# Optimization experiments

Hardware: AMD Instinct MI355X
Metric: run time of the kernel (lower is better)

The kernel has to match this reference:

```python
import jax, jax.numpy as jnp
import numpy as np

N_PAPER, N_MESH = 60000, 30000
N = N_PAPER + N_MESH
E_TRAIN, E_DEC = 2000000, 400000
F_PAPER = F_MESH = 128
D0, H, D = 16, 32, 16  # initial embed, hidden, final embed
NREL, NB = 2, 4


def _glorot(key, shape):
    fan_in, fan_out = shape[-2], shape[-1]
    s = jnp.sqrt(6.0 / (fan_in + fan_out)).astype(jnp.float32)
    return jax.random.uniform(key, shape, jnp.float32, -s, s)


def setup_inputs() -> dict:
    key = jax.random.key(0)
    ks = iter(jax.random.split(key, 40))
    inp = {
        'x_paper': jax.random.normal(next(ks), (N_PAPER, F_PAPER), jnp.float32),
        'x_mesh': jax.random.normal(next(ks), (N_MESH, F_MESH), jnp.float32),
        'train_edge_index': jax.random.randint(next(ks), (2, E_TRAIN), 0, N, jnp.int64 if jax.config.jax_enable_x64 else jnp.int32),
        'train_edge_type': jnp.sort(jax.random.randint(next(ks), (E_TRAIN,), 0, NREL)),
        'pos_edge_index': jax.random.randint(next(ks), (2, E_DEC), 0, N),
        'pos_edge_type': jnp.sort(jax.random.randint(next(ks), (E_DEC,), 0, NREL)),
        'neg_edge_index': jax.random.randint(next(ks), (2, E_DEC), 0, N),
        'neg_edge_type': jnp.sort(jax.random.randint(next(ks), (E_DEC,), 0, NREL)),
        # input transforms
        'Wp': _glorot(next(ks), (F_PAPER, D0)), 'bp': jnp.zeros((D0,), jnp.float32),
        'Wm': _glorot(next(ks), (F_MESH, D0)), 'bm': jnp.zeros((D0,), jnp.float32),
        # decode linears
        'Wd0': _glorot(next(ks), (D, D)), 'bd0': jnp.zeros((D,), jnp.float32),
        'Wd1': _glorot(next(ks), (D, D)), 'bd1': jnp.zeros((D,), jnp.float32),
    }
    dims = [(D0, H), (H, H), (H, H), (H, D)]
    for i, (di, do) in enumerate(dims, 1):
        inp[f'bases{i}'] = _glorot(next(ks), (NB, di, do))
        inp[f'comp{i}'] = _glorot(next(ks), (NREL, NB))
        inp[f'root{i}'] = _glorot(next(ks), (di, do))
        inp[f'bias{i}'] = jnp.zeros((do,), jnp.float32)
    return inp


def rgcn_layer(x, src, dst, et, bases, comp, root, bias):
    # PyG RGCNConv with basis decomposition, per-relation mean aggregation.
    out = x @ root + bias
    xs = x[src]  # [E, in]
    for r in range(NREL):
        W_r = jnp.einsum('b,bio->io', comp[r], bases)
        m = xs @ W_r  # [E, out]
        mf = (et == r).astype(m.dtype)
        cnt = jax.ops.segment_sum(mf, dst, num_segments=N)
        agg = jax.ops.segment_sum(m * mf[:, None], dst, num_segments=N)
        out = out + agg / jnp.clip(cnt, 1.0)[:, None]
    return out


def _decode_block(z, ei, et, Wd0, bd0, Wd1, bd1):
    zs, zd = z[ei[0]], z[ei[1]]
    h0 = zs @ Wd0 + bd0
    h1 = zs @ Wd1 + bd1
    h = jnp.where((et == 0)[:, None], h0, h1)
    return jnp.sum(h * zd, axis=-1)


def reference(x_paper, x_mesh, train_edge_index, train_edge_type,
              pos_edge_index, pos_edge_type, neg_edge_index, neg_edge_type,
              Wp, bp, Wm, bm, Wd0, bd0, Wd1, bd1,
              bases1, comp1, root1, bias1, bases2, comp2, root2, bias2,
              bases3, comp3, root3, bias3, bases4, comp4, root4, bias4):
    x = jnp.concatenate([x_paper @ Wp + bp, x_mesh @ Wm + bm], axis=0)  # [N, D0]
    src, dst = train_edge_index[0], train_edge_index[1]
    x = jax.nn.relu(rgcn_layer(x, src, dst, train_edge_type, bases1, comp1, root1, bias1))
    x = jax.nn.relu(rgcn_layer(x, src, dst, train_edge_type, bases2, comp2, root2, bias2))
    x = jax.nn.relu(rgcn_layer(x, src, dst, train_edge_type, bases3, comp3, root3, bias3))
    z = rgcn_layer(x, src, dst, train_edge_type, bases4, comp4, root4, bias4)
    # edge types are sorted, so per-edge in-order compute matches the masked concat order
    pos = _decode_block(z, pos_edge_index, pos_edge_type, Wd0, bd0, Wd1, bd1)
    neg = _decode_block(z, neg_edge_index, neg_edge_type, Wd0, bd0, Wd1, bd1)
    return jnp.concatenate([pos, neg], axis=0)  # [2*E_DEC]
```

## Files before the change

kernel.cpp:

```cpp
#include <hip/hip_runtime.h>
#include <hip/hip_bf16.h>

constexpr int NN = 90000;
constexpr int NP = 60000;
constexpr int NM = 30000;
constexpr int ET = 2000000;
constexpr int ED = 400000;
constexpr int TWO_NN = 2 * NN;

constexpr int BKT_SH  = 9;
constexpr int NB_BKT  = (TWO_NN + 511) >> BKT_SH;
constexpr int BKT_CAP = 6400;
constexpr int TILE    = 2048;
constexpr int N_TILES = (ET + TILE - 1) / TILE;

__device__ __forceinline__ float bflo(unsigned int u) {
    union { unsigned int i; float f; } c;
    c.i = u << 16;
    return c.f;
}
__device__ __forceinline__ float bfhi(unsigned int u) {
    union { unsigned int i; float f; } c;
    c.i = u & 0xffff0000u;
    return c.f;
}
__device__ __forceinline__ unsigned short f2bf(float f) {
    union { float f; unsigned int i; } c;
    c.f = f;
    unsigned int x = c.i;
    return (unsigned short)((x + 0x7FFFu + ((x >> 16) & 1u)) >> 16);
}

__global__ void init_kernel(const int* __restrict__ tei, int* __restrict__ gcur,
                            int* __restrict__ dflag) {
    int b = blockIdx.x * blockDim.x + threadIdx.x;
    if (b < NB_BKT) gcur[b] = b * BKT_CAP;
    if (b == 0) {
        int allzero = 1;
        for (int i = 0; i < 16; i++)
            if (tei[2 * i + 1] != 0) allzero = 0;
        dflag[0] = allzero;
    }
}

__global__ void __launch_bounds__(256) binA_kernel(
        const int* __restrict__ ei, const int* __restrict__ et,
        const int* __restrict__ dflag, int* __restrict__ gcur,
        int2* __restrict__ pairs) {
    __shared__ int histw[4][NB_BKT];
    __shared__ int wbase[4][NB_BKT];
    __shared__ int tot[NB_BKT];
    __shared__ int excl[NB_BKT];
    __shared__ int gbase[NB_BKT];
    __shared__ int scn[256];
    __shared__ int2 tbuf[TILE];
    int t = threadIdx.x;
    int w = t >> 6;
    int tile0 = blockIdx.x * TILE;
    int tcount = ET - tile0;
    if (tcount > TILE) tcount = TILE;
    for (int i = t; i < 4 * NB_BKT; i += 256) ((int*)histw)[i] = 0;
    __syncthreads();
    int sft = dflag[0];
    int myk[8], mys[8];
#pragma unroll
    for (int q = 0; q < 8; q++) {
        int li = q * 256 + t;
        myk[q] = -1;
        if (li < tcount) {
            int e = tile0 + li;
            int s = ei[(size_t)e << sft];
            int d = ei[(size_t)(ET + e) << sft];
            int r = et[(size_t)e << sft];
            int key = r * NN + d;
            myk[q] = key;
            mys[q] = s;
            atomicAdd(&histw[w][key >> BKT_SH], 1);
        }
    }
    __syncthreads();
    for (int i = t; i < NB_BKT; i += 256) {
        int h0 = histw[0][i], h1 = histw[1][i], h2 = histw[2][i], h3 = histw[3][i];
        wbase[0][i] = 0;
        wbase[1][i] = h0;
        wbase[2][i] = h0 + h1;
        wbase[3][i] = h0 + h1 + h2;
        tot[i] = h0 + h1 + h2 + h3;
    }
    __syncthreads();
    int v0 = (t < NB_BKT / 2) ? tot[2 * t] : 0;
    int v1 = (t < NB_BKT / 2) ? tot[2 * t + 1] : 0;
    int s = v0 + v1;
    scn[t] = s;
    __syncthreads();
    for (int st = 1; st < 256; st <<= 1) {
        int u = (t >= st) ? scn[t - st] : 0;
        __syncthreads();
        scn[t] += u;
        __syncthreads();
    }
    int base = scn[t] - s;
    if (t < NB_BKT / 2) {
        excl[2 * t] = base;
        excl[2 * t + 1] = base + v0;
    }
    __syncthreads();
    for (int i = t; i < NB_BKT; i += 256) {
        int e0 = excl[i];
        wbase[0][i] += e0;
        wbase[1][i] += e0;
        wbase[2][i] += e0;
        wbase[3][i] += e0;
        histw[0][i] = 0; histw[1][i] = 0; histw[2][i] = 0; histw[3][i] = 0;
    }
    __syncthreads();
#pragma unroll
    for (int q = 0; q < 8; q++) {
        if (myk[q] >= 0) {
            int b = myk[q] >> BKT_SH;
            int p = wbase[w][b] + atomicAdd(&histw[w][b], 1);
            tbuf[p] = make_int2(myk[q], mys[q]);
        }
    }
    __syncthreads();
    for (int i = t; i < NB_BKT; i += 256)
        if (tot[i] > 0) gbase[i] = atomicAdd(&gcur[i], tot[i]);
    __syncthreads();
    for (int i = t; i < tcount; i += 256) {
        int2 p = tbuf[i];
        int b = p.x >> BKT_SH;
        int gpos = gbase[b] + (i - excl[b]);
        int cap = (b + 1) * BKT_CAP - 1;
        pairs[gpos < cap ? gpos : cap] = p;
    }
}

__global__ void __launch_bounds__(256) histplace_kernel(
        const int* __restrict__ gcur, const int2* __restrict__ pairs,
        int* __restrict__ off, int* __restrict__ endo, float* __restrict__ inv,
        int* __restrict__ csr) {
    __shared__ int kh[512];
    __shared__ int scn[256];
    int b = blockIdx.x;
    int t = threadIdx.x;
    int beg = b * BKT_CAP, end = gcur[b];
    for (int i = t; i < 512; i += 256) kh[i] = 0;
    __syncthreads();
    for (int i = beg + t; i < end; i += 256)
        atomicAdd(&kh[pairs[i].x & 511], 1);
    __syncthreads();
    int v[2];
    int s = 0;
#pragma unroll
    for (int q = 0; q < 2; q++) {
        v[q] = kh[t * 2 + q];
        s += v[q];
    }
    scn[t] = s;
    __syncthreads();
    for (int st = 1; st < 256; st <<= 1) {
        int u = (t >= st) ? scn[t - st] : 0;
        __syncthreads();
        scn[t] += u;
        __syncthreads();
    }
    int run = beg + scn[t] - s;
    int kbase = b << BKT_SH;
    int kc[2];
#pragma unroll
    for (int q = 0; q < 2; q++) {
        int key = kbase + t * 2 + q;
        if (key < TWO_NN) {
            off[key] = run;
            endo[key] = run + v[q];
            inv[key] = 1.0f / (float)(v[q] > 1 ? v[q] : 1);
        }
        kc[q] = run;
        run += v[q];
    }
    __syncthreads();
#pragma unroll
    for (int q = 0; q < 2; q++) kh[t * 2 + q] = kc[q];
    __syncthreads();
    for (int i = beg + t; i < end; i += 256) {
        int2 p = pairs[i];
        int pos = atomicAdd(&kh[p.x & 511], 1);
        csr[pos] = p.y;
    }
}

__global__ void __launch_bounds__(256) embed2_kernel(
        const float* __restrict__ Xp, const float* __restrict__ Xm,
        const float* __restrict__ Wp, const float* __restrict__ bp,
        const float* __restrict__ Wm, const float* __restrict__ bm,
        unsigned short* __restrict__ outbf) {
    __shared__ float Wl[4096 + 32];
    for (int i = threadIdx.x; i < 2048; i += 256) {
        Wl[i] = Wp[i];
        Wl[2048 + i] = Wm[i];
    }
    if (threadIdx.x < 16) {
        Wl[4096 + threadIdx.x] = bp[threadIdx.x];
        Wl[4112 + threadIdx.x] = bm[threadIdx.x];
    }
    __syncthreads();
    int n = blockIdx.x * 256 + threadIdx.x;
    if (n >= NN) return;
    const float* X;
    const float* Ws;
    const float* Bs;
    if (n < NP) { X = Xp + (size_t)n * 128; Ws = Wl; Bs = Wl + 4096; }
    else        { X = Xm + (size_t)(n - NP) * 128; Ws = Wl + 2048; Bs = Wl + 4112; }
    float acc[16];
#pragma unroll
    for (int j = 0; j < 16; j++) acc[j] = Bs[j];
    const float4* row = (const float4*)X;
    for (int k4 = 0; k4 < 32; k4++) {
        float4 xv = row[k4];
        int k = k4 * 4;
#pragma unroll
        for (int j = 0; j < 16; j++) {
            float a = acc[j];
            a = fmaf(xv.x, Ws[(k + 0) * 16 + j], a);
            a = fmaf(xv.y, Ws[(k + 1) * 16 + j], a);
            a = fmaf(xv.z, Ws[(k + 2) * 16 + j], a);
            a = fmaf(xv.w, Ws[(k + 3) * 16 + j], a);
            acc[j] = a;
        }
    }
    ushort4* ob = (ushort4*)(outbf + (size_t)n * 16);
#pragma unroll
    for (int q = 0; q < 4; q++) {
        ushort4 ub;
        ub.x = f2bf(acc[4 * q]);     ub.y = f2bf(acc[4 * q + 1]);
        ub.z = f2bf(acc[4 * q + 2]); ub.w = f2bf(acc[4 * q + 3]);
        ob[q] = ub;
    }
}

__global__ void prep_all_kernel(
        const float* __restrict__ ba0, const float* __restrict__ co0,
        const float* __restrict__ ro0, const float* __restrict__ bi0,
        const float* __restrict__ ba1, const float* __restrict__ co1,
        const float* __restrict__ ro1, const float* __restrict__ bi1,
        const float* __restrict__ ba2, const float* __restrict__ co2,
        const float* __restrict__ ro2, const float* __restrict__ bi2,
        const float* __restrict__ ba3, const float* __restrict__ co3,
        const float* __restrict__ ro3, const float* __restrict__ bi3,
        float* __restrict__ Wbuf4) {
    int l = blockIdx.x;
    const float* bases; const float* comp; const float* root; const float* bias;
    if (l == 0)      { bases = ba0; comp = co0; root = ro0; bias = bi0; }
    else if (l == 1) { bases = ba1; comp = co1; root = ro1; bias = bi1; }
    else if (l == 2) { bases = ba2; comp = co2; root = ro2; bias = bi2; }
    else             { bases = ba3; comp = co3; root = ro3; bias = bi3; }
    int din = (l == 0) ? 16 : 32;
    int dout = (l == 3) ? 16 : 32;
    int sz = din * dout;
    float* W = Wbuf4 + l * 3200;
    for (int i = threadIdx.x; i < sz; i += 256) {
        float b0 = bases[i];
        float b1 = bases[sz + i];
        float b2 = bases[2 * sz + i];
        float b3 = bases[3 * sz + i];
        for (int r = 0; r < 2; r++) {
            W[r * sz + i] = comp[r * 4 + 0] * b0 + comp[r * 4 + 1] * b1 +
                            comp[r * 4 + 2] * b2 + comp[r * 4 + 3] * b3;
        }
        W[2 * sz + i] = root[i];
    }
    if (threadIdx.x < dout) W[3 * sz + threadIdx.x] = bias[threadIdx.x];
}

template <int DIN, int DOUT, int RELU, int BS>
__global__ void __launch_bounds__(BS, 8) layer_kernel(
        const int* __restrict__ off, const int* __restrict__ endo,
        const int* __restrict__ csr,
        const unsigned short* __restrict__ xbf_in,
        const float* __restrict__ inv, const float* __restrict__ Wbuf,
        unsigned short* __restrict__ xbf_out) {
    constexpr int SZ = DIN * DOUT;
    constexpr int QL = DIN / 8;
    constexpr int TPN = 2 * QL;
    constexpr int NPB = BS / TPN;
    constexpr int AGST = 2 * DIN + 4;
    constexpr int XSST = DIN + 8;
    __shared__ float Wl[3 * SZ + DOUT];
    __shared__ float agg[NPB * AGST];
    __shared__ unsigned short xsu[NPB * XSST];
    for (int i = threadIdx.x; i < 3 * SZ + DOUT; i += BS) Wl[i] = Wbuf[i];
    int t = threadIdx.x;
    int ln = t / TPN;
    int rl = t % TPN;
    int r = rl / QL;
    int lane = rl % QL;
    int d = blockIdx.x * NPB + ln;
    if (d < NN) {
        if (r == 0) {
            uint4 u = *(const uint4*)(xbf_in + (size_t)d * DIN + lane * 8);
            *(uint4*)&xsu[ln * XSST + lane * 8] = u;
        }
        int key = r * NN + d;
        int b = off[key];
        int e = endo[key];
        float a0[8] = {0, 0, 0, 0, 0, 0, 0, 0};
        float a1[8] = {0, 0, 0, 0, 0, 0, 0, 0};
        const unsigned short* hp = xbf_in + lane * 8;
        int k = b;
        for (; k + 1 < e; k += 2) {
            int s0 = __builtin_nontemporal_load(csr + k);
            int s1 = __builtin_nontemporal_load(csr + k + 1);
            uint4 u0 = *(const uint4*)(hp + (size_t)s0 * DIN);
            uint4 u1 = *(const uint4*)(hp + (size_t)s1 * DIN);
            a0[0] += bflo(u0.x); a0[1] += bfhi(u0.x);
            a0[2] += bflo(u0.y); a0[3] += bfhi(u0.y);
            a0[4] += bflo(u0.z); a0[5] += bfhi(u0.z);
            a0[6] += bflo(u0.w); a0[7] += bfhi(u0.w);
            a1[0] += bflo(u1.x); a1[1] += bfhi(u1.x);
            a1[2] += bflo(u1.y); a1[3] += bfhi(u1.y);
            a1[4] += bflo(u1.z); a1[5] += bfhi(u1.z);
            a1[6] += bflo(u1.w); a1[7] += bfhi(u1.w);
        }
        if (k < e) {
            int s0 = __builtin_nontemporal_load(csr + k);
            uint4 u0 = *(const uint4*)(hp + (size_t)s0 * DIN);
            a0[0] += bflo(u0.x); a0[1] += bfhi(u0.x);
            a0[2] += bflo(u0.y); a0[3] += bfhi(u0.y);
            a0[4] += bflo(u0.z); a0[5] += bfhi(u0.z);
            a0[6] += bflo(u0.w); a0[7] += bfhi(u0.w);
        }
        float* ap = agg + ln * AGST + r * DIN + lane * 8;
        *(float4*)ap = make_float4(a0[0] + a1[0], a0[1] + a1[1],
                                   a0[2] + a1[2], a0[3] + a1[3]);
        *(float4*)(ap + 4) = make_float4(a0[4] + a1[4], a0[5] + a1[5],
                                         a0[6] + a1[6], a0[7] + a1[7]);
    }
    __syncthreads();
    constexpr int CPN = DOUT / 4;
    for (int tt = t; tt < NPB * CPN; tt += BS) {
        int ln2 = tt / CPN;
        int j0 = (tt % CPN) * 4;
        int d2 = blockIdx.x * NPB + ln2;
        if (d2 < NN) {
            float iv0 = inv[d2], iv1 = inv[NN + d2];
            float acc[4];
#pragma unroll
            for (int jj = 0; jj < 4; jj++) acc[jj] = Wl[3 * SZ + j0 + jj];
#pragma unroll
            for (int k2 = 0; k2 < DIN; k2 += 2) {
                unsigned up = *(const unsigned*)&xsu[ln2 * XSST + k2];
                float xv0 = bflo(up);
                float xv1 = bfhi(up);
                float m00 = agg[ln2 * AGST + k2] * iv0;
                float m10 = agg[ln2 * AGST + DIN + k2] * iv1;
                float m01 = agg[ln2 * AGST + k2 + 1] * iv0;
                float m11 = agg[ln2 * AGST + DIN + k2 + 1] * iv1;
                const float* w0a = &Wl[k2 * DOUT + j0];
                const float* w1a = &Wl[SZ + k2 * DOUT + j0];
                const float* wra = &Wl[2 * SZ + k2 * DOUT + j0];
#pragma unroll
                for (int jj = 0; jj < 4; jj++) {
                    acc[jj] = fmaf(xv0, wra[jj], acc[jj]);
                    acc[jj] = fmaf(m00, w0a[jj], acc[jj]);
                    acc[jj] = fmaf(m10, w1a[jj], acc[jj]);
                    acc[jj] = fmaf(xv1, wra[DOUT + jj], acc[jj]);
                    acc[jj] = fmaf(m01, w0a[DOUT + jj], acc[jj]);
                    acc[jj] = fmaf(m11, w1a[DOUT + jj], acc[jj]);
                }
            }
            if (RELU) {
#pragma unroll
                for (int jj = 0; jj < 4; jj++) acc[jj] = fmaxf(acc[jj], 0.0f);
            }
            ushort4 ub;
            ub.x = f2bf(acc[0]); ub.y = f2bf(acc[1]);
            ub.z = f2bf(acc[2]); ub.w = f2bf(acc[3]);
            union { ushort4 v; unsigned long long q; } pk;
            pk.v = ub;
            __builtin_nontemporal_store(
                pk.q, (unsigned long long*)(xbf_out + (size_t)d2 * DOUT + j0));
        }
    }
}

__global__ void __launch_bounds__(256) decode_fused_kernel(
        const unsigned short* __restrict__ zbf,
        const float* __restrict__ Wd0, const float* __restrict__ bd0,
        const float* __restrict__ Wd1, const float* __restrict__ bd1,
        const int* __restrict__ pei, const int* __restrict__ pet,
        const int* __restrict__ nei, const int* __restrict__ net_,
        float* __restrict__ out, const int* __restrict__ dflag) {
    __shared__ float W[2][256];
    __shared__ float B[2][16];
    for (int i = threadIdx.x; i < 256; i += 256) {
        W[0][i] = Wd0[i];
        W[1][i] = Wd1[i];
    }
    if (threadIdx.x < 16) {
        B[0][threadIdx.x] = bd0[threadIdx.x];
        B[1][threadIdx.x] = bd1[threadIdx.x];
    }
    __syncthreads();
    int i = blockIdx.x * 256 + threadIdx.x;
    if (i >= 2 * ED) return;
    int sft = dflag[0];
    const int* ei;
    const int* et;
    int e;
    if (i < ED) { ei = pei; et = pet; e = i; }
    else        { ei = nei; et = net_; e = i - ED; }
    int s = ei[(size_t)e << sft];
    int d = ei[(size_t)(ED + e) << sft];
    int r = et[(size_t)e << sft];
    float zs[16], zd[16];
    const uint4* sp = (const uint4*)(zbf + ((size_t)s << 4));
    const uint4* dp = (const uint4*)(zbf + ((size_t)d << 4));
#pragma unroll
    for (int h = 0; h < 2; h++) {
        uint4 us = sp[h];
        uint4 ud = dp[h];
        int o8 = h * 8;
        zs[o8 + 0] = bflo(us.x); zs[o8 + 1] = bfhi(us.x);
        zs[o8 + 2] = bflo(us.y); zs[o8 + 3] = bfhi(us.y);
        zs[o8 + 4] = bflo(us.z); zs[o8 + 5] = bfhi(us.z);
        zs[o8 + 6] = bflo(us.w); zs[o8 + 7] = bfhi(us.w);
        zd[o8 + 0] = bflo(ud.x); zd[o8 + 1] = bfhi(ud.x);
        zd[o8 + 2] = bflo(ud.y); zd[o8 + 3] = bfhi(ud.y);
        zd[o8 + 4] = bflo(ud.z); zd[o8 + 5] = bfhi(ud.z);
        zd[o8 + 6] = bflo(ud.w); zd[o8 + 7] = bfhi(ud.w);
    }
    const float* Wr = W[r];
    const float* Br = B[r];
    float acc = 0.0f;
#pragma unroll
    for (int j = 0; j < 16; j++) {
        float yj = Br[j];
#pragma unroll
        for (int k = 0; k < 16; k++) yj = fmaf(zs[k], Wr[k * 16 + j], yj);
        acc = fmaf(yj, zd[j], acc);
    }
    out[i] = acc;
}

extern "C" void kernel_launch(void* const* d_in, const int* in_sizes, int n_in,
                              void* d_out, int out_size, void* d_ws, size_t ws_size,
                              hipStream_t stream) {
    const float* x_paper = (const float*)d_in[0];
    const float* x_mesh  = (const float*)d_in[1];
    const int* tei  = (const int*)d_in[2];
    const int* tet  = (const int*)d_in[3];
    const int* pei  = (const int*)d_in[4];
    const int* pet  = (const int*)d_in[5];
    const int* nei  = (const int*)d_in[6];
    const int* net_ = (const int*)d_in[7];
    const float* Wp  = (const float*)d_in[8];
    const float* bp  = (const float*)d_in[9];
    const float* Wm  = (const float*)d_in[10];
    const float* bm  = (const float*)d_in[11];
    const float* Wd0 = (const float*)d_in[12];
    const float* bd0 = (const float*)d_in[13];
    const float* Wd1 = (const float*)d_in[14];
    const float* bd1 = (const float*)d_in[15];

    float* ws = (float*)d_ws;
    size_t o = 0;
    unsigned short* xbfA = (unsigned short*)(ws + o); o += (size_t)NN * 16;
    unsigned short* xbfB = (unsigned short*)(ws + o); o += (size_t)NN * 16;
    float* inv  = ws + o; o += (size_t)TWO_NN;
    int*   off  = (int*)(ws + o); o += (size_t)TWO_NN;
    int*   endo = (int*)(ws + o); o += (size_t)TWO_NN;
    int*   csr  = (int*)(ws + o); o += (size_t)NB_BKT * BKT_CAP;
    int*   gcur = (int*)(ws + o); o += 512;
    int2*  pairs = (int2*)(ws + o); o += (size_t)2 * NB_BKT * BKT_CAP;
    float* Wbuf4 = ws + o; o += 4 * 3200;
    int*   dflag = (int*)(ws + o); o += 16;

    init_kernel<<<(NB_BKT + 255) / 256, 256, 0, stream>>>(tei, gcur, dflag);

    binA_kernel<<<N_TILES, 256, 0, stream>>>(tei, tet, dflag, gcur, pairs);
    histplace_kernel<<<NB_BKT, 256, 0, stream>>>(gcur, pairs, off, endo, inv, csr);

    embed2_kernel<<<(NN + 255) / 256, 256, 0, stream>>>(
        x_paper, x_mesh, Wp, bp, Wm, bm, xbfA);

    prep_all_kernel<<<4, 256, 0, stream>>>(
        (const float*)d_in[16], (const float*)d_in[17], (const float*)d_in[18], (const float*)d_in[19],
        (const float*)d_in[20], (const float*)d_in[21], (const float*)d_in[22], (const float*)d_in[23],
        (const float*)d_in[24], (const float*)d_in[25], (const float*)d_in[26], (const float*)d_in[27],
        (const float*)d_in[28], (const float*)d_in[29], (const float*)d_in[30], (const float*)d_in[31],
        Wbuf4);

    constexpr int LBS = 512;
    int blk16 = (NN + 127) / 128;
    int blk32 = (NN + 63) / 64;
    layer_kernel<16, 32, 1, LBS><<<blk16, LBS, 0, stream>>>(
        off, endo, csr, xbfA, inv, Wbuf4 + 0 * 3200, xbfB);
    layer_kernel<32, 32, 1, LBS><<<blk32, LBS, 0, stream>>>(
        off, endo, csr, xbfB, inv, Wbuf4 + 1 * 3200, xbfA);
    layer_kernel<32, 32, 1, LBS><<<blk32, LBS, 0, stream>>>(
        off, endo, csr, xbfA, inv, Wbuf4 + 2 * 3200, xbfB);
    layer_kernel<32, 16, 0, LBS><<<blk32, LBS, 0, stream>>>(
        off, endo, csr, xbfB, inv, Wbuf4 + 3 * 3200, xbfA);

    decode_fused_kernel<<<(2 * ED + 255) / 256, 256, 0, stream>>>(
        xbfA, Wd0, bd0, Wd1, bd1, pei, pet, nei, net_, (float*)d_out, dflag);
}
```

Measured before the change: 399.2 us.

## Software-pipeline CSR gather in RGCN layers, shrink blocks to 256 threads

The neighbor gather loop in the layer kernel is restructured to process four edges per iteration, prefetching the next four source indices while the current rows are loaded, so more loads are in flight per thread. Block size is cut from 512 to 256 threads with the 8-blocks occupancy hint removed, and grid sizes are doubled to match. Nontemporal hints on index loads and output stores are dropped in favor of plain accesses. The larger unroll raises register use and may lower occupancy; smaller blocks reload the weight tile into shared memory more often.

```diff
diff --git a/kernel.cpp b/kernel.cpp
--- a/kernel.cpp
+++ b/kernel.cpp
@@ -272,8 +272,8 @@
     if (threadIdx.x < dout) W[3 * sz + threadIdx.x] = bias[threadIdx.x];
 }
 
-template <int DIN, int DOUT, int RELU, int BS>
-__global__ void __launch_bounds__(BS, 8) layer_kernel(
+template <int DIN, int DOUT, int RELU>
+__global__ void __launch_bounds__(256) layer_kernel(
         const int* __restrict__ off, const int* __restrict__ endo,
         const int* __restrict__ csr,
         const unsigned short* __restrict__ xbf_in,
@@ -282,13 +282,13 @@
     constexpr int SZ = DIN * DOUT;
     constexpr int QL = DIN / 8;
     constexpr int TPN = 2 * QL;
-    constexpr int NPB = BS / TPN;
+    constexpr int NPB = 256 / TPN;
     constexpr int AGST = 2 * DIN + 4;
     constexpr int XSST = DIN + 8;
     __shared__ float Wl[3 * SZ + DOUT];
     __shared__ float agg[NPB * AGST];
     __shared__ unsigned short xsu[NPB * XSST];
-    for (int i = threadIdx.x; i < 3 * SZ + DOUT; i += BS) Wl[i] = Wbuf[i];
+    for (int i = threadIdx.x; i < 3 * SZ + DOUT; i += 256) Wl[i] = Wbuf[i];
     int t = threadIdx.x;
     int ln = t / TPN;
     int rl = t % TPN;
@@ -307,11 +307,37 @@
         float a1[8] = {0, 0, 0, 0, 0, 0, 0, 0};
         const unsigned short* hp = xbf_in + lane * 8;
         int k = b;
-        for (; k + 1 < e; k += 2) {
-            int s0 = __builtin_nontemporal_load(csr + k);
-            int s1 = __builtin_nontemporal_load(csr + k + 1);
+        if (k + 3 < e) {
+            int s0 = csr[k], s1 = csr[k + 1], s2 = csr[k + 2], s3 = csr[k + 3];
+            k += 4;
+            while (k + 3 < e) {
+                uint4 u0 = *(const uint4*)(hp + (size_t)s0 * DIN);
+                uint4 u1 = *(const uint4*)(hp + (size_t)s1 * DIN);
+                uint4 u2 = *(const uint4*)(hp + (size_t)s2 * DIN);
+                uint4 u3 = *(const uint4*)(hp + (size_t)s3 * DIN);
+                s0 = csr[k]; s1 = csr[k + 1]; s2 = csr[k + 2]; s3 = csr[k + 3];
+                k += 4;
+                a0[0] += bflo(u0.x); a0[1] += bfhi(u0.x);
+                a0[2] += bflo(u0.y); a0[3] += bfhi(u0.y);
+                a0[4] += bflo(u0.z); a0[5] += bfhi(u0.z);
+                a0[6] += bflo(u0.w); a0[7] += bfhi(u0.w);
+                a1[0] += bflo(u1.x); a1[1] += bfhi(u1.x);
+                a1[2] += bflo(u1.y); a1[3] += bfhi(u1.y);
+                a1[4] += bflo(u1.z); a1[5] += bfhi(u1.z);
+                a1[6] += bflo(u1.w); a1[7] += bfhi(u1.w);
+                a0[0] += bflo(u2.x); a0[1] += bfhi(u2.x);
+                a0[2] += bflo(u2.y); a0[3] += bfhi(u2.y);
+                a0[4] += bflo(u2.z); a0[5] += bfhi(u2.z);
+                a0[6] += bflo(u2.w); a0[7] += bfhi(u2.w);
+                a1[0] += bflo(u3.x); a1[1] += bfhi(u3.x);
+                a1[2] += bflo(u3.y); a1[3] += bfhi(u3.y);
+                a1[4] += bflo(u3.z); a1[5] += bfhi(u3.z);
+                a1[6] += bflo(u3.w); a1[7] += bfhi(u3.w);
+            }
             uint4 u0 = *(const uint4*)(hp + (size_t)s0 * DIN);
             uint4 u1 = *(const uint4*)(hp + (size_t)s1 * DIN);
+            uint4 u2 = *(const uint4*)(hp + (size_t)s2 * DIN);
+            uint4 u3 = *(const uint4*)(hp + (size_t)s3 * DIN);
             a0[0] += bflo(u0.x); a0[1] += bfhi(u0.x);
             a0[2] += bflo(u0.y); a0[3] += bfhi(u0.y);
             a0[4] += bflo(u0.z); a0[5] += bfhi(u0.z);
@@ -320,10 +346,17 @@
             a1[2] += bflo(u1.y); a1[3] += bfhi(u1.y);
             a1[4] += bflo(u1.z); a1[5] += bfhi(u1.z);
             a1[6] += bflo(u1.w); a1[7] += bfhi(u1.w);
-        }
-        if (k < e) {
-            int s0 = __builtin_nontemporal_load(csr + k);
-            uint4 u0 = *(const uint4*)(hp + (size_t)s0 * DIN);
+            a0[0] += bflo(u2.x); a0[1] += bfhi(u2.x);
+            a0[2] += bflo(u2.y); a0[3] += bfhi(u2.y);
+            a0[4] += bflo(u2.z); a0[5] += bfhi(u2.z);
+            a0[6] += bflo(u2.w); a0[7] += bfhi(u2.w);
+            a1[0] += bflo(u3.x); a1[1] += bfhi(u3.x);
+            a1[2] += bflo(u3.y); a1[3] += bfhi(u3.y);
+            a1[4] += bflo(u3.z); a1[5] += bfhi(u3.z);
+            a1[6] += bflo(u3.w); a1[7] += bfhi(u3.w);
+        }
+        for (; k < e; k++) {
+            uint4 u0 = *(const uint4*)(hp + (size_t)csr[k] * DIN);
             a0[0] += bflo(u0.x); a0[1] += bfhi(u0.x);
             a0[2] += bflo(u0.y); a0[3] += bfhi(u0.y);
             a0[4] += bflo(u0.z); a0[5] += bfhi(u0.z);
@@ -337,7 +370,7 @@
     }
     __syncthreads();
     constexpr int CPN = DOUT / 4;
-    for (int tt = t; tt < NPB * CPN; tt += BS) {
+    for (int tt = t; tt < NPB * CPN; tt += 256) {
         int ln2 = tt / CPN;
         int j0 = (tt % CPN) * 4;
         int d2 = blockIdx.x * NPB + ln2;
@@ -375,10 +408,7 @@
             ushort4 ub;
             ub.x = f2bf(acc[0]); ub.y = f2bf(acc[1]);
             ub.z = f2bf(acc[2]); ub.w = f2bf(acc[3]);
-            union { ushort4 v; unsigned long long q; } pk;
-            pk.v = ub;
-            __builtin_nontemporal_store(
-                pk.q, (unsigned long long*)(xbf_out + (size_t)d2 * DOUT + j0));
+            *(ushort4*)(xbf_out + (size_t)d2 * DOUT + j0) = ub;
         }
     }
 }
@@ -490,16 +520,15 @@
         (const float*)d_in[28], (const float*)d_in[29], (const float*)d_in[30], (const float*)d_in[31],
         Wbuf4);
 
-    constexpr int LBS = 512;
-    int blk16 = (NN + 127) / 128;
-    int blk32 = (NN + 63) / 64;
-    layer_kernel<16, 32, 1, LBS><<<blk16, LBS, 0, stream>>>(
+    int blk16 = (NN + 63) / 64;
+    int blk32 = (NN + 31) / 32;
+    layer_kernel<16, 32, 1><<<blk16, 256, 0, stream>>>(
         off, endo, csr, xbfA, inv, Wbuf4 + 0 * 3200, xbfB);
-    layer_kernel<32, 32, 1, LBS><<<blk32, LBS, 0, stream>>>(
+    layer_kernel<32, 32, 1><<<blk32, 256, 0, stream>>>(
         off, endo, csr, xbfB, inv, Wbuf4 + 1 * 3200, xbfA);
-    layer_kernel<32, 32, 1, LBS><<<blk32, LBS, 0, stream>>>(
+    layer_kernel<32, 32, 1><<<blk32, 256, 0, stream>>>(
         off, endo, csr, xbfA, inv, Wbuf4 + 2 * 3200, xbfB);
-    layer_kernel<32, 16, 0, LBS><<<blk32, LBS, 0, stream>>>(
+    layer_kernel<32, 16, 0><<<blk32, 256, 0, stream>>>(
         off, endo, csr, xbfB, inv, Wbuf4 + 3 * 3200, xbfA);
 
     decode_fused_kernel<<<(2 * ED + 255) / 256, 256, 0, stream>>>(
```

After: 355.6 us. 10.9% less time.
